# Optimization experiments

Hardware: AMD Instinct MI355X
Metric: run time of the kernel (lower is better)

## Reference

```python
import jax
import jax.numpy as jnp
from jax import lax
import numpy as np

B, C, H, W = 32, 256, 64, 64
R = 16  # low-rank dim of random bias


def setup_inputs() -> dict:
    key = jax.random.key(0)
    ks = jax.random.split(key, 6)
    return {
        "x": jax.random.normal(ks[0], (B, C, H, W), dtype=jnp.float32),
        "x_mid": jax.random.normal(ks[1], (B, C, H, W), dtype=jnp.float32),
        "g_w": jax.random.normal(ks[2], (C, C, 3, 3), dtype=jnp.float32) * 0.02,
        "w_w": jax.random.normal(ks[3], (C, C, 1, 1), dtype=jnp.float32) * 0.02,
        "weight1": jax.random.normal(ks[4], (C, R), dtype=jnp.float32) * 0.1,
        "weight2": jax.random.normal(ks[5], (C, R), dtype=jnp.float32) * 0.1,
    }


def _conv(x, w, padding):
    return lax.conv_general_dilated(
        x, w, window_strides=(1, 1), padding=padding,
        dimension_numbers=("NCHW", "OIHW", "NCHW"))


def reference(x, x_mid, g_w, w_w, weight1, weight2):
    b, c, h, w = x.shape
    # value path: 3x3 conv on x_mid (padding 1 -> SAME)
    g_x = _conv(x_mid, g_w, "SAME")                       # [b,c,h,w]
    value = g_x.reshape(b, c, h * w)                       # [b,c,N]
    feats = x.reshape(b, c, h * w)                         # query == key == x
    # channel-channel similarity: [b,c,c]
    sim = jnp.einsum("bcn,bdn->bcd", feats, feats) * (c ** -0.5)
    random_map = weight1 @ weight2.T                        # [c,c] low-rank bias
    attn = jax.nn.softmax(sim + random_map[None, :, :], axis=-1)
    context = jnp.einsum("bcd,bdn->bcn", attn, value).reshape(b, c, h, w)
    return _conv(context, w_w, "VALID")                     # 1x1 conv
```

## Files before the change

kernel.cpp:

```cpp
#include <hip/hip_runtime.h>


#define NB 32
#define NC 256
#define NPIX 4096
#define KSPLIT 4

typedef __attribute__((ext_vector_type(8))) short short8;
typedef __attribute__((ext_vector_type(16))) float floatx16;

__device__ inline short f2bf(float f) {
    union { float f; unsigned u; } v; v.f = f;
    unsigned r = v.u + 0x7fffu + ((v.u >> 16) & 1u);
    return (short)(r >> 16);
}

__global__ __launch_bounds__(256) void rm_kernel(const float* __restrict__ w1,
                                                 const float* __restrict__ w2,
                                                 float* __restrict__ rm) {
    int idx = blockIdx.x * 256 + threadIdx.x;
    int c = idx >> 8, d = idx & 255;
    float s = 0.f;
#pragma unroll
    for (int r = 0; r < 16; r++) s += w1[c * 16 + r] * w2[d * 16 + r];
    rm[idx] = s;
}

__global__ __launch_bounds__(256) void cvt_bf16_kernel(const float* __restrict__ in,
                                                       short* __restrict__ out) {
    size_t i = ((size_t)blockIdx.x * 256 + threadIdx.x) * 8;
    float4 v0 = *(const float4*)&in[i];
    float4 v1 = *(const float4*)&in[i + 4];
    short8 s;
    s[0] = f2bf(v0.x); s[1] = f2bf(v0.y); s[2] = f2bf(v0.z); s[3] = f2bf(v0.w);
    s[4] = f2bf(v1.x); s[5] = f2bf(v1.y); s[6] = f2bf(v1.z); s[7] = f2bf(v1.w);
    *(short8*)&out[i] = s;
}

__global__ __launch_bounds__(256) void cvt_x_kernel(const float* __restrict__ x,
                                                    short* __restrict__ xt) {
    const int h = blockIdx.x;
    const int b = blockIdx.y;
    __shared__ short xls[64 * 256];
    const int tid = threadIdx.x;
    for (int i = tid; i < 4096; i += 256) {
        int ci = i >> 4, w4 = (i & 15) << 2;
        float4 v = *(const float4*)&x[(((size_t)(b * 256 + ci)) * 64 + h) * 64 + w4];
        xls[(w4 + 0) * 256 + ci] = f2bf(v.x);
        xls[(w4 + 1) * 256 + ci] = f2bf(v.y);
        xls[(w4 + 2) * 256 + ci] = f2bf(v.z);
        xls[(w4 + 3) * 256 + ci] = f2bf(v.w);
    }
    __syncthreads();
    uint4* dst = (uint4*)&xt[(((size_t)(b * 64 + h)) * 64) * 256];
    const uint4* src = (const uint4*)xls;
    for (int i = tid; i < 2048; i += 256) dst[i] = src[i];
}

__global__ __launch_bounds__(256) void cvt_w_kernel(const float* __restrict__ g_w,
                                                    short* __restrict__ wt) {
    int o = blockIdx.x * 256 + threadIdx.x;
    if (o >= 73728) return;
    int co_t = o / 18432;
    int rem  = o - co_t * 18432;
    int ci_b = rem / 1152;
    int rem2 = rem - ci_b * 1152;
    int tap  = rem2 / 128;
    int rem3 = rem2 - tap * 128;
    int ch   = rem3 >> 6, ls = rem3 & 63;
    int co = co_t * 64 + ch * 32 + (ls & 31);
    int ci0 = ci_b * 16 + (ls >> 5) * 8;
    short8 v;
#pragma unroll
    for (int j = 0; j < 8; j++)
        v[j] = f2bf(g_w[((size_t)co * 256 + ci0 + j) * 9 + tap]);
    *(short8*)&wt[(size_t)o * 8] = v;
}

__global__ __launch_bounds__(256) void conv_mfma(const short* __restrict__ xt,
                                                 const short* __restrict__ wt,
                                                 short* __restrict__ value_t) {
    const int h0  = blockIdx.x * 4;
    const int cot = blockIdx.y;
    const int b   = blockIdx.z;
    __shared__ short ws[9 * 2 * 64 * 8];
    __shared__ short xs[6 * 2 * 66 * 8];
    const int tid = threadIdx.x;
    const int wv = tid >> 6, lane = tid & 63;
    const int kh2 = lane >> 5, ln = lane & 31;

    int xr0, xw0, xh0_, xr1, xw1, xh1_, xr2, xw2, xh2_;
    {
        int i0 = tid;        xr0 = i0 >> 7; int r0 = i0 & 127; xw0 = r0 >> 1; xh0_ = r0 & 1;
        int i1 = tid + 256;  xr1 = i1 >> 7; int r1 = i1 & 127; xw1 = r1 >> 1; xh1_ = r1 & 1;
        int i2 = tid + 512;  xr2 = i2 >> 7; int r2 = i2 & 127; xw2 = r2 >> 1; xh2_ = r2 & 1;
    }
    const int xd0 = (xr0 * 2 + xh0_) * 66 + 1 + xw0;
    const int xd1 = (xr1 * 2 + xh1_) * 66 + 1 + xw1;
    const int xd2 = (xr2 * 2 + xh2_) * 66 + 1 + xw2;
    const int hin0 = h0 - 1 + xr0, hin1 = h0 - 1 + xr1, hin2 = h0 - 1 + xr2;
    const uint4* wsrc_base = (const uint4*)&wt[(size_t)(cot * 16) * 1152 * 8];

    uint4 wr0, wr1, wr2, wr3, wr4;
    uint4 xv0, xv1, xv2;

#define LOAD_CIB(c)                                                            \
    do {                                                                       \
        const uint4* wsrc = wsrc_base + (size_t)(c) * 1152;                    \
        wr0 = wsrc[tid];        wr1 = wsrc[tid + 256];                         \
        wr2 = wsrc[tid + 512];  wr3 = wsrc[tid + 768];                         \
        if (tid < 128) wr4 = wsrc[tid + 1024];                                 \
        xv0 = make_uint4(0, 0, 0, 0); xv1 = xv0; xv2 = xv0;                    \
        if ((unsigned)hin0 < 64u)                                              \
            xv0 = *(const uint4*)&xt[(((size_t)(b * 64 + hin0)) * 64 + xw0) * 256 + (c) * 16 + xh0_ * 8]; \
        if ((unsigned)hin1 < 64u)                                              \
            xv1 = *(const uint4*)&xt[(((size_t)(b * 64 + hin1)) * 64 + xw1) * 256 + (c) * 16 + xh1_ * 8]; \
        if ((unsigned)hin2 < 64u)                                              \
            xv2 = *(const uint4*)&xt[(((size_t)(b * 64 + hin2)) * 64 + xw2) * 256 + (c) * 16 + xh2_ * 8]; \
    } while (0)

#define WRITE_LDS()                                                            \
    do {                                                                       \
        uint4* wdst = (uint4*)ws;                                              \
        wdst[tid] = wr0;        wdst[tid + 256] = wr1;                         \
        wdst[tid + 512] = wr2;  wdst[tid + 768] = wr3;                         \
        if (tid < 128) wdst[tid + 1024] = wr4;                                 \
        uint4* xdst = (uint4*)xs;                                              \
        xdst[xd0] = xv0; xdst[xd1] = xv1; xdst[xd2] = xv2;                     \
    } while (0)

    if (tid < 24) {
        int r = tid >> 2, half = (tid >> 1) & 1, side = tid & 1;
        ((uint4*)xs)[(r * 2 + half) * 66 + side * 65] = make_uint4(0, 0, 0, 0);
    }

    floatx16 acc00 = {}, acc01 = {}, acc10 = {}, acc11 = {};

    LOAD_CIB(0);
    for (int cib = 0; cib < 16; ++cib) {
        __syncthreads();
        WRITE_LDS();
        if (cib < 15) LOAD_CIB(cib + 1);
        __syncthreads();

#pragma unroll
        for (int tap = 0; tap < 9; ++tap) {
            const int kh = tap / 3, kw = tap - kh * 3;
            const int r = wv + kh;
            short8 wf0 = *(const short8*)&ws[((tap * 2 + 0) * 64 + lane) * 8];
            short8 wf1 = *(const short8*)&ws[((tap * 2 + 1) * 64 + lane) * 8];
            short8 xf0 = *(const short8*)&xs[(((r * 2 + kh2) * 66) + kw + ln) * 8];
            short8 xf1 = *(const short8*)&xs[(((r * 2 + kh2) * 66) + kw + 32 + ln) * 8];
            acc00 = __builtin_amdgcn_mfma_f32_32x32x16_bf16(xf0, wf0, acc00, 0, 0, 0);
            acc01 = __builtin_amdgcn_mfma_f32_32x32x16_bf16(xf0, wf1, acc01, 0, 0, 0);
            acc10 = __builtin_amdgcn_mfma_f32_32x32x16_bf16(xf1, wf0, acc10, 0, 0, 0);
            acc11 = __builtin_amdgcn_mfma_f32_32x32x16_bf16(xf1, wf1, acc11, 0, 0, 0);
        }
    }
#undef LOAD_CIB
#undef WRITE_LDS

    const int h_out = h0 + wv;
    short* vt = value_t + ((size_t)(b * 4096 + h_out * 64)) * 256 + cot * 64;
#pragma unroll
    for (int reg = 0; reg < 16; ++reg) {
        int m = (reg & 3) + 8 * (reg >> 2) + 4 * kh2;
        vt[(size_t)m * 256 + ln]             = f2bf(acc00[reg]);
        vt[(size_t)m * 256 + 32 + ln]        = f2bf(acc01[reg]);
        vt[(size_t)(m + 32) * 256 + ln]      = f2bf(acc10[reg]);
        vt[(size_t)(m + 32) * 256 + 32 + ln] = f2bf(acc11[reg]);
    }
}

__global__ __launch_bounds__(128) void gemm_nt_bf16(const short* __restrict__ A,
                                                    const short* __restrict__ B,
                                                    float* __restrict__ C,
                                                    int Kld, int Ksub,
                                                    long sA, long sB, long sC,
                                                    int ldc, int tilesN, int tilesXY,
                                                    long sKsl) {
    const int kslice = blockIdx.x / tilesXY;
    const int t = blockIdx.x - kslice * tilesXY;
    const int mt = t / tilesN, nt = t - (t / tilesN) * tilesN;
    A += (size_t)blockIdx.y * sA;
    B += (size_t)blockIdx.y * sB;
    C += (size_t)blockIdx.y * sC + (size_t)kslice * sKsl;
    const int wv = threadIdx.x >> 6, l = threadIdx.x & 63;
    const int ln = l & 31, kh = l >> 5;
    const int kbase = kslice * Ksub;
    const short* arow = A + (size_t)(mt * 64 + wv * 32 + ln) * Kld + kbase + kh * 8;
    const short* brow = B + (size_t)(nt * 128 + ln) * Kld + kbase + kh * 8;
    floatx16 acc0 = {}, acc1 = {}, acc2 = {}, acc3 = {};
#pragma unroll 2
    for (int k0 = 0; k0 < Ksub; k0 += 16) {
        short8 a  = *(const short8*)&arow[k0];
        short8 b0 = *(const short8*)&brow[k0];
        short8 b1 = *(const short8*)&brow[(size_t)32 * Kld + k0];
        short8 b2 = *(const short8*)&brow[(size_t)64 * Kld + k0];
        short8 b3 = *(const short8*)&brow[(size_t)96 * Kld + k0];
        acc0 = __builtin_amdgcn_mfma_f32_32x32x16_bf16(a, b0, acc0, 0, 0, 0);
        acc1 = __builtin_amdgcn_mfma_f32_32x32x16_bf16(a, b1, acc1, 0, 0, 0);
        acc2 = __builtin_amdgcn_mfma_f32_32x32x16_bf16(a, b2, acc2, 0, 0, 0);
        acc3 = __builtin_amdgcn_mfma_f32_32x32x16_bf16(a, b3, acc3, 0, 0, 0);
    }
    const int n0 = nt * 128;
#pragma unroll
    for (int reg = 0; reg < 16; ++reg) {
        int m = mt * 64 + wv * 32 + (reg & 3) + 8 * (reg >> 2) + 4 * kh;
        float* crow = C + (size_t)m * ldc + n0 + ln;
        crow[0]  = acc0[reg];
        crow[32] = acc1[reg];
        crow[64] = acc2[reg];
        crow[96] = acc3[reg];
    }
}

template <int BT, int OB>
__global__ __launch_bounds__(256) void gemm64(const float* __restrict__ A,
                                              const float* __restrict__ B,
                                              float* __restrict__ C, int K,
                                              long sA, long sB, long sC,
                                              int ldA, int ldB, int ldC, int tilesN) {
    const int m0 = (blockIdx.x / tilesN) * 64;
    const int n0 = (blockIdx.x % tilesN) * 64;
    A += (size_t)blockIdx.y * sA;
    B += (size_t)blockIdx.y * sB;
    const size_t coff = (size_t)blockIdx.y * sC;
    __shared__ float As[16][68], Bs[16][68];
    const int tid = threadIdx.x;
    const int tx = tid & 15, ty = tid >> 4;
    const int mm = tid >> 2, kk4 = (tid & 3) * 4;
    float acc[4][4] = {};

    for (int k0 = 0; k0 < K; k0 += 16) {
        __syncthreads();
        {
            float4 a = *(const float4*)&A[(size_t)(m0 + mm) * ldA + k0 + kk4];
            As[kk4 + 0][mm] = a.x; As[kk4 + 1][mm] = a.y;
            As[kk4 + 2][mm] = a.z; As[kk4 + 3][mm] = a.w;
        }
        if (BT) {
            float4 bv = *(const float4*)&B[(size_t)(n0 + mm) * ldB + k0 + kk4];
            Bs[kk4 + 0][mm] = bv.x; Bs[kk4 + 1][mm] = bv.y;
            Bs[kk4 + 2][mm] = bv.z; Bs[kk4 + 3][mm] = bv.w;
        } else {
            int bk = tid >> 4, bn = (tid & 15) * 4;
            *(float4*)&Bs[bk][bn] = *(const float4*)&B[(size_t)(k0 + bk) * ldB + n0 + bn];
        }
        __syncthreads();
#pragma unroll
        for (int kk = 0; kk < 16; kk++) {
            float4 a = *(float4*)&As[kk][ty * 4];
            float4 bv = *(float4*)&Bs[kk][tx * 4];
            float av[4] = {a.x, a.y, a.z, a.w};
            float bb[4] = {bv.x, bv.y, bv.z, bv.w};
#pragma unroll
            for (int i = 0; i < 4; i++)
#pragma unroll
                for (int j = 0; j < 4; j++) acc[i][j] += av[i] * bb[j];
        }
    }
#pragma unroll
    for (int i = 0; i < 4; i++) {
        if (OB) {
            short* Cs = (short*)C + coff;
            short4 o;
            o.x = f2bf(acc[i][0]); o.y = f2bf(acc[i][1]);
            o.z = f2bf(acc[i][2]); o.w = f2bf(acc[i][3]);
            *(short4*)&Cs[(size_t)(m0 + ty * 4 + i) * ldC + n0 + tx * 4] = o;
        } else {
            float* Cf = (float*)C + coff;
            float4 o = make_float4(acc[i][0], acc[i][1], acc[i][2], acc[i][3]);
            *(float4*)&Cf[(size_t)(m0 + ty * 4 + i) * ldC + n0 + tx * 4] = o;
        }
    }
}

__global__ __launch_bounds__(256) void softmax_kernel(float* __restrict__ sim,
                                                      const float* __restrict__ part,
                                                      const float* __restrict__ rm) {
    int row  = blockIdx.x * 4 + (threadIdx.x >> 6);
    int lane = threadIdx.x & 63;
    int c = row & 255;
    const size_t off = (size_t)row * 256 + lane * 4;
    const size_t sP = (size_t)NB * NC * NC;
    float4 v  = *(const float4*)&part[off];
    float4 p1 = *(const float4*)&part[off + sP];
    float4 p2 = *(const float4*)&part[off + 2 * sP];
    float4 p3 = *(const float4*)&part[off + 3 * sP];
    v.x += p1.x + p2.x + p3.x;
    v.y += p1.y + p2.y + p3.y;
    v.z += p1.z + p2.z + p3.z;
    v.w += p1.w + p2.w + p3.w;
    const float4 bias = *(const float4*)&rm[c * 256 + lane * 4];
    v.x = v.x * 0.0625f + bias.x;
    v.y = v.y * 0.0625f + bias.y;
    v.z = v.z * 0.0625f + bias.z;
    v.w = v.w * 0.0625f + bias.w;
    float m = fmaxf(fmaxf(v.x, v.y), fmaxf(v.z, v.w));
#pragma unroll
    for (int off2 = 32; off2 > 0; off2 >>= 1) m = fmaxf(m, __shfl_xor(m, off2, 64));
    float e0 = __expf(v.x - m), e1 = __expf(v.y - m);
    float e2 = __expf(v.z - m), e3 = __expf(v.w - m);
    float s = e0 + e1 + e2 + e3;
#pragma unroll
    for (int off2 = 32; off2 > 0; off2 >>= 1) s += __shfl_xor(s, off2, 64);
    float inv = 1.f / s;
    float4 o = make_float4(e0 * inv, e1 * inv, e2 * inv, e3 * inv);
    *(float4*)&sim[off] = o;
}

extern "C" void kernel_launch(void* const* d_in, const int* in_sizes, int n_in,
                              void* d_out, int out_size, void* d_ws, size_t ws_size,
                              hipStream_t stream) {
    const float* x     = (const float*)d_in[0];
    const float* x_mid = (const float*)d_in[1];
    const float* g_w   = (const float*)d_in[2];
    const float* w_w   = (const float*)d_in[3];
    const float* w1    = (const float*)d_in[4];
    const float* w2    = (const float*)d_in[5];
    float* out = (float*)d_out;

    char* ws = (char*)d_ws;
    short* value_t = (short*)ws;
    float* sim     = (float*)(ws + (size_t)NB * NPIX * NC * 2);
    short* attn2_b = (short*)(sim + (size_t)NB * NC * NC);
    float* rm      = (float*)(attn2_b + (size_t)NB * NC * NC);
    short* xt      = (short*)(rm + NC * NC);
    short* xb      = xt + (size_t)NB * NPIX * NC;
    short* wt      = xb + (size_t)NB * NC * NPIX;

    float* simPart = out;

    cvt_w_kernel<<<288, 256, 0, stream>>>(g_w, wt);
    cvt_x_kernel<<<dim3(64, 32), 256, 0, stream>>>(x_mid, xt);
    cvt_bf16_kernel<<<16384, 256, 0, stream>>>(x, xb);
    rm_kernel<<<256, 256, 0, stream>>>(w1, w2, rm);
    conv_mfma<<<dim3(16, 4, 32), 256, 0, stream>>>(xt, wt, value_t);
    gemm_nt_bf16<<<dim3(8 * KSPLIT, 32), 128, 0, stream>>>(
        xb, xb, simPart, 4096, 4096 / KSPLIT,
        (long)NC * NPIX, (long)NC * NPIX, (long)NC * NC, NC, 2, 8,
        (long)NB * NC * NC);
    softmax_kernel<<<2048, 256, 0, stream>>>(sim, simPart, rm);
    gemm64<0, 1><<<dim3(16, 32), 256, 0, stream>>>(
        w_w, sim, (float*)attn2_b, 256,
        0L, (long)NC * NC, (long)NC * NC,
        NC, NC, NC, 4);
    gemm_nt_bf16<<<dim3(128, 32), 128, 0, stream>>>(
        attn2_b, value_t, out, 256, 256,
        (long)NC * NC, (long)NPIX * NC, (long)NC * NPIX, NPIX, 32, 128, 0L);
}
```

Before: 703.8 us.

## Stream conv weights directly to registers and double-buffer input tile in LDS

The 3x3 conv MFMA kernel no longer stages weights through shared memory. Each wave streams its weight fragments from global memory into a small rotating register buffer, prefetched a few taps ahead. The input tile gets two LDS buffers, which removes one of the two barriers per channel block. The intent is to cut LDS traffic and synchronisation, at the cost of more global/L2 weight reads (every wave reloads the same weights) and extra register pressure.

```diff
diff --git a/kernel.cpp b/kernel.cpp
--- a/kernel.cpp
+++ b/kernel.cpp
@@ -83,8 +83,7 @@
     const int h0  = blockIdx.x * 4;
     const int cot = blockIdx.y;
     const int b   = blockIdx.z;
-    __shared__ short ws[9 * 2 * 64 * 8];
-    __shared__ short xs[6 * 2 * 66 * 8];
+    __shared__ short xs[2][6 * 2 * 66 * 8];
     const int tid = threadIdx.x;
     const int wv = tid >> 6, lane = tid & 63;
     const int kh2 = lane >> 5, ln = lane & 31;
@@ -99,17 +98,16 @@
     const int xd1 = (xr1 * 2 + xh1_) * 66 + 1 + xw1;
     const int xd2 = (xr2 * 2 + xh2_) * 66 + 1 + xw2;
     const int hin0 = h0 - 1 + xr0, hin1 = h0 - 1 + xr1, hin2 = h0 - 1 + xr2;
-    const uint4* wsrc_base = (const uint4*)&wt[(size_t)(cot * 16) * 1152 * 8];
-
-    uint4 wr0, wr1, wr2, wr3, wr4;
+
+    const uint4* wsrc = (const uint4*)&wt[(size_t)(cot * 16) * 1152 * 8];
+
+    uint4 wbuf[6];
+#pragma unroll
+    for (int s = 0; s < 6; ++s) wbuf[s] = wsrc[(size_t)s * 64 + lane];
+
     uint4 xv0, xv1, xv2;
-
-#define LOAD_CIB(c)                                                            \
+#define LOAD_X(c)                                                              \
     do {                                                                       \
-        const uint4* wsrc = wsrc_base + (size_t)(c) * 1152;                    \
-        wr0 = wsrc[tid];        wr1 = wsrc[tid + 256];                         \
-        wr2 = wsrc[tid + 512];  wr3 = wsrc[tid + 768];                         \
-        if (tid < 128) wr4 = wsrc[tid + 1024];                                 \
         xv0 = make_uint4(0, 0, 0, 0); xv1 = xv0; xv2 = xv0;                    \
         if ((unsigned)hin0 < 64u)                                              \
             xv0 = *(const uint4*)&xt[(((size_t)(b * 64 + hin0)) * 64 + xw0) * 256 + (c) * 16 + xh0_ * 8]; \
@@ -119,46 +117,47 @@
             xv2 = *(const uint4*)&xt[(((size_t)(b * 64 + hin2)) * 64 + xw2) * 256 + (c) * 16 + xh2_ * 8]; \
     } while (0)
 
-#define WRITE_LDS()                                                            \
-    do {                                                                       \
-        uint4* wdst = (uint4*)ws;                                              \
-        wdst[tid] = wr0;        wdst[tid + 256] = wr1;                         \
-        wdst[tid + 512] = wr2;  wdst[tid + 768] = wr3;                         \
-        if (tid < 128) wdst[tid + 1024] = wr4;                                 \
-        uint4* xdst = (uint4*)xs;                                              \
-        xdst[xd0] = xv0; xdst[xd1] = xv1; xdst[xd2] = xv2;                     \
-    } while (0)
-
     if (tid < 24) {
         int r = tid >> 2, half = (tid >> 1) & 1, side = tid & 1;
-        ((uint4*)xs)[(r * 2 + half) * 66 + side * 65] = make_uint4(0, 0, 0, 0);
-    }
+        int o = (r * 2 + half) * 66 + side * 65;
+        ((uint4*)xs[0])[o] = make_uint4(0, 0, 0, 0);
+        ((uint4*)xs[1])[o] = make_uint4(0, 0, 0, 0);
+    }
+
+    LOAD_X(0);
 
     floatx16 acc00 = {}, acc01 = {}, acc10 = {}, acc11 = {};
 
-    LOAD_CIB(0);
     for (int cib = 0; cib < 16; ++cib) {
+        {
+            uint4* xdst = (uint4*)xs[cib & 1];
+            xdst[xd0] = xv0; xdst[xd1] = xv1; xdst[xd2] = xv2;
+        }
         __syncthreads();
-        WRITE_LDS();
-        if (cib < 15) LOAD_CIB(cib + 1);
-        __syncthreads();
-
+        if (cib < 15) LOAD_X(cib + 1);
+
+        const short* xsc = xs[cib & 1];
 #pragma unroll
         for (int tap = 0; tap < 9; ++tap) {
             const int kh = tap / 3, kw = tap - kh * 3;
             const int r = wv + kh;
-            short8 wf0 = *(const short8*)&ws[((tap * 2 + 0) * 64 + lane) * 8];
-            short8 wf1 = *(const short8*)&ws[((tap * 2 + 1) * 64 + lane) * 8];
-            short8 xf0 = *(const short8*)&xs[(((r * 2 + kh2) * 66) + kw + ln) * 8];
-            short8 xf1 = *(const short8*)&xs[(((r * 2 + kh2) * 66) + kw + 32 + ln) * 8];
+            const int slot = (tap % 3) * 2;
+            short8 wf0 = __builtin_bit_cast(short8, wbuf[slot]);
+            short8 wf1 = __builtin_bit_cast(short8, wbuf[slot + 1]);
+            int sp = cib * 18 + tap * 2 + 6;
+            int sp0 = sp     > 287 ? 287 : sp;
+            int sp1 = sp + 1 > 287 ? 287 : sp + 1;
+            wbuf[slot]     = wsrc[(size_t)sp0 * 64 + lane];
+            wbuf[slot + 1] = wsrc[(size_t)sp1 * 64 + lane];
+            short8 xf0 = *(const short8*)&xsc[(((r * 2 + kh2) * 66) + kw + ln) * 8];
+            short8 xf1 = *(const short8*)&xsc[(((r * 2 + kh2) * 66) + kw + 32 + ln) * 8];
             acc00 = __builtin_amdgcn_mfma_f32_32x32x16_bf16(xf0, wf0, acc00, 0, 0, 0);
             acc01 = __builtin_amdgcn_mfma_f32_32x32x16_bf16(xf0, wf1, acc01, 0, 0, 0);
             acc10 = __builtin_amdgcn_mfma_f32_32x32x16_bf16(xf1, wf0, acc10, 0, 0, 0);
             acc11 = __builtin_amdgcn_mfma_f32_32x32x16_bf16(xf1, wf1, acc11, 0, 0, 0);
         }
     }
-#undef LOAD_CIB
-#undef WRITE_LDS
+#undef LOAD_X
 
     const int h_out = h0 + wv;
     short* vt = value_t + ((size_t)(b * 4096 + h_out * 64)) * 256 + cot * 64;
```

New measurement: 747.7 us. 1.06x slower.
